# Optimization experiments

Hardware: AMD Instinct MI355X
Metric: run time of the kernel (lower is better)

The kernel has to match this reference:

```python
import jax, jax.numpy as jnp
import numpy as np

B, S, H = 16, 512, 768
NH, HD = 12, 64  # num heads, head dim


def setup_inputs() -> dict:
    key = jax.random.key(0)
    ks = jax.random.split(key, 7)
    std = 0.02
    return {
        "hidden_state": jax.random.normal(ks[0], (B, S, H), dtype=jnp.float32),
        "attention_mask": jnp.ones((B, S), dtype=jnp.float32),
        "Wq": jax.random.normal(ks[1], (H, H), dtype=jnp.float32) * std,
        "bq": jnp.zeros((H,), dtype=jnp.float32),
        "Wk": jax.random.normal(ks[2], (H, H), dtype=jnp.float32) * std,
        "bk": jnp.zeros((H,), dtype=jnp.float32),
        "Wv": jax.random.normal(ks[3], (H, H), dtype=jnp.float32) * std,
        "bv": jnp.zeros((H,), dtype=jnp.float32),
    }


def reference(hidden_state, attention_mask, Wq, bq, Wk, bk, Wv, bv):
    b, s, h = hidden_state.shape
    scale = 1.0 / jnp.sqrt(jnp.asarray(HD, hidden_state.dtype))

    def split_heads(x):  # [B,S,H] -> [B,NH,S,HD]
        return x.reshape(b, s, NH, HD).transpose(0, 2, 1, 3)

    q = split_heads(hidden_state @ Wq.T + bq)
    k = split_heads(hidden_state @ Wk.T + bk)
    v = split_heads(hidden_state @ Wv.T + bv)

    # [B,NH,S,S]
    scores = jnp.einsum("bhqd,bhkd->bhqk", q, k) * scale
    mask_add = (1.0 - attention_mask)[:, None, None, :] * -10000.0
    probs = jax.nn.softmax(scores + mask_add, axis=-1)
    # dropout is identity in eval / deterministic reference

    ctx = jnp.einsum("bhqk,bhkd->bhqd", probs, v)
    ctx = ctx.transpose(0, 2, 1, 3).reshape(b, s, NH * HD)
    return ctx, probs
```

## Files before the change

kernel.cpp:

```cpp
#include <hip/hip_runtime.h>

namespace {
constexpr int kB  = 16;
constexpr int kS  = 512;
constexpr int kH  = 768;
constexpr int kNH = 12;
constexpr int kHD = 64;
constexpr int kM  = kB * kS;
}

typedef __attribute__((ext_vector_type(8))) short  short8;
typedef __attribute__((ext_vector_type(4))) float  f32x4;
typedef __attribute__((ext_vector_type(4))) unsigned short us4;
typedef __attribute__((ext_vector_type(2))) unsigned int   u32x2;

__device__ __forceinline__ unsigned short f2bf(float x) {
    unsigned u = __float_as_uint(x);
    return (unsigned short)((u + 0x7FFFu + ((u >> 16) & 1u)) >> 16);
}

__device__ __forceinline__ unsigned pack_bf16(float lo, float hi) {
    return (unsigned)f2bf(lo) | ((unsigned)f2bf(hi) << 16);
}

__device__ __forceinline__ void load_lds16(const unsigned short* g, unsigned short* l) {
    __builtin_amdgcn_global_load_lds(
        (const __attribute__((address_space(1))) void*)g,
        (__attribute__((address_space(3))) void*)l,
        16, 0, 0);
}

__global__ __launch_bounds__(256) void cvt_all_kernel(
    const float* __restrict__ hidden, const float* __restrict__ Wq,
    const float* __restrict__ Wk, const float* __restrict__ Wv,
    unsigned short* __restrict__ hbf, unsigned short* __restrict__ wqb,
    unsigned short* __restrict__ wkb, unsigned short* __restrict__ wvb)
{
    const int nH4 = (kM * kH) / 4;
    const int nW4 = (kH * kH) / 4;
    int i = blockIdx.x * 256 + threadIdx.x;
    const float* src;
    unsigned short* dst;
    int off;
    if (i < nH4) {
        src = hidden; dst = hbf; off = i;
    } else {
        int j = i - nH4;
        int which = j / nW4;
        off = j - which * nW4;
        src = (which == 0) ? Wq : (which == 1) ? Wk : Wv;
        dst = (which == 0) ? wqb : (which == 1) ? wkb : wvb;
    }
    float4 v = reinterpret_cast<const float4*>(src)[off];
    us4 o;
    o.x = f2bf(v.x); o.y = f2bf(v.y); o.z = f2bf(v.z); o.w = f2bf(v.w);
    reinterpret_cast<us4*>(dst)[off] = o;
}

__global__ __launch_bounds__(256) void qkv_mfma_kernel(
    const unsigned short* __restrict__ hbf,
    const unsigned short* __restrict__ Wqb,
    const unsigned short* __restrict__ Wkb,
    const unsigned short* __restrict__ Wvb,
    const float* __restrict__ bq, const float* __restrict__ bk,
    const float* __restrict__ bv,
    unsigned short* __restrict__ qhi, unsigned short* __restrict__ qlo,
    unsigned short* __restrict__ khi, unsigned short* __restrict__ klo,
    unsigned short* __restrict__ vt)
{
    const int which = blockIdx.z;
    const unsigned short* W = (which == 0) ? Wqb : (which == 1) ? Wkb : Wvb;
    const float* bias       = (which == 0) ? bq  : (which == 1) ? bk  : bv;

    const int n0 = blockIdx.x * 128;
    const int m0 = blockIdx.y * 128;

    const int t    = threadIdx.x;
    const int lane = t & 63;
    const int w    = t >> 6;
    const int wm   = w >> 1;
    const int wn   = w & 1;

    __shared__ unsigned short As[128 * 64];
    __shared__ unsigned short Bs[128 * 64];

    f32x4 acc[4][4] = {};

    const int row8  = lane >> 3;
    const int sunit = (lane & 7) ^ row8;
    const unsigned short* gA = hbf + (size_t)(m0 + w * 32 + row8) * kH + sunit * 8;
    const unsigned short* gB = W   + (size_t)(n0 + w * 32 + row8) * kH + sunit * 8;

    const int frow = lane & 15;
    const int fk   = (lane >> 4) * 8;
    const int fswz = (frow & 7) << 3;

    for (int k0 = 0; k0 < kH; k0 += 64) {
#pragma unroll
        for (int i = 0; i < 4; ++i) {
            load_lds16(gA + k0 + (size_t)(8 * i) * kH, &As[(w * 32 + 8 * i) * 64]);
            load_lds16(gB + k0 + (size_t)(8 * i) * kH, &Bs[(w * 32 + 8 * i) * 64]);
        }
        __syncthreads();

        short8 af[2][4], bf[2][4];
#pragma unroll
        for (int kk = 0; kk < 2; ++kk) {
#pragma unroll
            for (int i = 0; i < 4; ++i)
                af[kk][i] = *reinterpret_cast<const short8*>(
                    &As[(wm * 64 + i * 16 + frow) * 64 + ((kk * 32 + fk) ^ fswz)]);
#pragma unroll
            for (int j = 0; j < 4; ++j)
                bf[kk][j] = *reinterpret_cast<const short8*>(
                    &Bs[(wn * 64 + j * 16 + frow) * 64 + ((kk * 32 + fk) ^ fswz)]);
        }
#pragma unroll
        for (int kk = 0; kk < 2; ++kk)
#pragma unroll
            for (int i = 0; i < 4; ++i)
#pragma unroll
                for (int j = 0; j < 4; ++j)
                    acc[i][j] = __builtin_amdgcn_mfma_f32_16x16x32_bf16(
                        af[kk][i], bf[kk][j], acc[i][j], 0, 0, 0);
        __syncthreads();
    }

    const int col = lane & 15;
    const int rq4 = (lane >> 4) << 2;

    if (which < 2) {
        unsigned short* ohi = which ? khi : qhi;
        unsigned short* olo = which ? klo : qlo;
#pragma unroll
        for (int j = 0; j < 4; ++j) {
            const int n  = n0 + wn * 64 + j * 16 + col;
            const float bj = bias[n];
            const int hh = n >> 6, d = n & 63;
#pragma unroll
            for (int i = 0; i < 4; ++i) {
                const int mrow = m0 + wm * 64 + i * 16 + rq4;
                const int bb = mrow >> 9;
                const int ss = mrow & 511;
                const size_t base =
                    ((size_t)(bb * kNH + hh) * kS + ss) * kHD + d;
#pragma unroll
                for (int r = 0; r < 4; ++r) {
                    float x = acc[i][j][r] + bj;
                    unsigned short hi = f2bf(x);
                    float res = x - __uint_as_float((unsigned)hi << 16);
                    ohi[base + (size_t)r * kHD] = hi;
                    olo[base + (size_t)r * kHD] = f2bf(res);
                }
            }
        }
    } else {
#pragma unroll
        for (int j = 0; j < 4; ++j) {
            const int n  = n0 + wn * 64 + j * 16 + col;
            const float bj = bias[n];
            const int hh = n >> 6, d = n & 63;
#pragma unroll
            for (int i = 0; i < 4; ++i) {
                const int mrow = m0 + wm * 64 + i * 16 + rq4;
                const int bb = mrow >> 9;
                const int ss = mrow & 511;
                us4 o;
                o.x = f2bf(acc[i][j][0] + bj);
                o.y = f2bf(acc[i][j][1] + bj);
                o.z = f2bf(acc[i][j][2] + bj);
                o.w = f2bf(acc[i][j][3] + bj);
                *reinterpret_cast<us4*>(
                    &vt[((size_t)(bb * kNH + hh) * kHD + d) * kS + ss]) = o;
            }
        }
    }
}

__global__ __launch_bounds__(256) void attn_kernel(
    const unsigned short* __restrict__ qhi, const unsigned short* __restrict__ qlo,
    const unsigned short* __restrict__ khi, const unsigned short* __restrict__ klo,
    const unsigned short* __restrict__ vtp, const float* __restrict__ mask,
    float* __restrict__ ctx, float* __restrict__ probs)
{
    const int bid = blockIdx.x;
    const int swz = (bid & 7) * 192 + (bid >> 3);
    const int qt  = swz & 7;
    const int bh  = swz >> 3;
    const int b   = bh / kNH;
    const int h   = bh % kNH;
    const int q0  = qt * 64;

    const int t    = threadIdx.x;
    const int lane = t & 63;
    const int w    = t >> 6;
    const int g    = lane >> 4;
    const int fr   = lane & 15;

    __shared__ unsigned short Khs[2][4096];
    __shared__ unsigned short Kls[2][4096];
    __shared__ unsigned short Vts[2][4096];
    __shared__ unsigned int   Pp[4][576];

    const int qrow = q0 + w * 16 + fr;
    const unsigned short* qh = qhi + ((size_t)bh * kS + qrow) * kHD + g * 8;
    const unsigned short* ql = qlo + ((size_t)bh * kS + qrow) * kHD + g * 8;
    const short8 qfh0 = *reinterpret_cast<const short8*>(qh);
    const short8 qfh1 = *reinterpret_cast<const short8*>(qh + 32);
    const short8 qfl0 = *reinterpret_cast<const short8*>(ql);
    const short8 qfl1 = *reinterpret_cast<const short8*>(ql + 32);

    const int c0 = (w * 2 + 0) * 64 + lane;
    const int c1 = (w * 2 + 1) * 64 + lane;
    const int r0 = c0 >> 3, r1 = c1 >> 3;
    const int s0b = ((c0 & 7) * 16) ^ ((r0 & 7) << 4);
    const int s1b = ((c1 & 7) * 16) ^ ((r1 & 7) << 4);
    const int ko0 = r0 * 128 + s0b,  ko1 = r1 * 128 + s1b;
    const int vo0 = r0 * 1024 + s0b, vo1 = r1 * 1024 + s1b;
    const char* kh_b = (const char*)(khi + (size_t)bh * kS * kHD);
    const char* kl_b = (const char*)(klo + (size_t)bh * kS * kHD);
    const char* vt_b = (const char*)(vtp + (size_t)bh * kHD * kS);
    const int l0 = (w * 2 + 0) * 512;
    const int l1 = (w * 2 + 1) * 512;

    unsigned pk[8][4][2];
    f32x4 cacc[4] = {};
    float rs = 0.0f;
    const float* mrow = mask + b * kS;

    load_lds16((const unsigned short*)(kh_b + ko0), &Khs[0][l0]);
    load_lds16((const unsigned short*)(kh_b + ko1), &Khs[0][l1]);
    load_lds16((const unsigned short*)(kl_b + ko0), &Kls[0][l0]);
    load_lds16((const unsigned short*)(kl_b + ko1), &Kls[0][l1]);
    load_lds16((const unsigned short*)(vt_b + vo0), &Vts[0][l0]);
    load_lds16((const unsigned short*)(vt_b + vo1), &Vts[0][l1]);

#pragma unroll
    for (int kt = 0; kt < 8; ++kt) {
        const int cur = kt & 1;
        __syncthreads();

        if (kt < 7) {
            const int nxt = cur ^ 1;
            load_lds16((const unsigned short*)(kh_b + (kt + 1) * 8192 + ko0), &Khs[nxt][l0]);
            load_lds16((const unsigned short*)(kh_b + (kt + 1) * 8192 + ko1), &Khs[nxt][l1]);
            load_lds16((const unsigned short*)(kl_b + (kt + 1) * 8192 + ko0), &Kls[nxt][l0]);
            load_lds16((const unsigned short*)(kl_b + (kt + 1) * 8192 + ko1), &Kls[nxt][l1]);
            load_lds16((const unsigned short*)(vt_b + (kt + 1) * 128 + vo0), &Vts[nxt][l0]);
            load_lds16((const unsigned short*)(vt_b + (kt + 1) * 128 + vo1), &Vts[nxt][l1]);
        }

        __builtin_amdgcn_s_setprio(1);

#pragma unroll
        for (int ks = 0; ks < 4; ++ks) {
            f32x4 sa = {};
#pragma unroll
            for (int d2 = 0; d2 < 2; ++d2) {
                const int kr  = ks * 16 + fr;
                const int off = kr * 128 + ((d2 * 64 + g * 16) ^ ((kr & 7) << 4));
                short8 ah = *reinterpret_cast<const short8*>((const char*)Khs[cur] + off);
                short8 al = *reinterpret_cast<const short8*>((const char*)Kls[cur] + off);
                const short8 qhf = d2 ? qfh1 : qfh0;
                const short8 qlf = d2 ? qfl1 : qfl0;
                sa = __builtin_amdgcn_mfma_f32_16x16x32_bf16(ah, qhf, sa, 0, 0, 0);
                sa = __builtin_amdgcn_mfma_f32_16x16x32_bf16(ah, qlf, sa, 0, 0, 0);
                sa = __builtin_amdgcn_mfma_f32_16x16x32_bf16(al, qhf, sa, 0, 0, 0);
            }
            const float4 mv = *reinterpret_cast<const float4*>(
                &mrow[kt * 64 + ks * 16 + g * 4]);
            float p0 = __expf(fmaf(sa[0], 0.125f, fmaf(mv.x, 1e4f, -1e4f)));
            float p1 = __expf(fmaf(sa[1], 0.125f, fmaf(mv.y, 1e4f, -1e4f)));
            float p2 = __expf(fmaf(sa[2], 0.125f, fmaf(mv.z, 1e4f, -1e4f)));
            float p3 = __expf(fmaf(sa[3], 0.125f, fmaf(mv.w, 1e4f, -1e4f)));
            rs += (p0 + p1) + (p2 + p3);
            const unsigned u0 = pack_bf16(p0, p1);
            const unsigned u1 = pack_bf16(p2, p3);
            pk[kt][ks][0] = u0;
            pk[kt][ks][1] = u1;
            *reinterpret_cast<u32x2*>(&Pp[w][fr * 36 + ks * 8 + g * 2]) =
                (u32x2){u0, u1};
        }

#pragma unroll
        for (int kp = 0; kp < 2; ++kp) {
            short8 pa = *reinterpret_cast<const short8*>(
                &Pp[w][fr * 36 + kp * 16 + g * 4]);
#pragma unroll
            for (int dt = 0; dt < 4; ++dt) {
                const int vr  = dt * 16 + fr;
                const int off = vr * 128 + ((kp * 64 + g * 16) ^ ((vr & 7) << 4));
                short8 vb = *reinterpret_cast<const short8*>((const char*)Vts[cur] + off);
                cacc[dt] = __builtin_amdgcn_mfma_f32_16x16x32_bf16(
                    pa, vb, cacc[dt], 0, 0, 0);
            }
        }

        __builtin_amdgcn_s_setprio(0);
    }

    rs += __shfl_xor(rs, 16, 64);
    rs += __shfl_xor(rs, 32, 64);
    const float inv = 1.0f / rs;

    float* prow = probs + ((size_t)bh * kS + qrow) * kS;
#pragma unroll
    for (int kt = 0; kt < 8; ++kt)
#pragma unroll
        for (int ks = 0; ks < 4; ++ks) {
            const unsigned u0 = pk[kt][ks][0], u1 = pk[kt][ks][1];
            f32x4 o;
            o.x = __uint_as_float(u0 << 16) * inv;
            o.y = __uint_as_float(u0 & 0xFFFF0000u) * inv;
            o.z = __uint_as_float(u1 << 16) * inv;
            o.w = __uint_as_float(u1 & 0xFFFF0000u) * inv;
            __builtin_nontemporal_store(
                o, reinterpret_cast<f32x4*>(prow + kt * 64 + ks * 16 + g * 4));
        }

    float invr[4];
#pragma unroll
    for (int r = 0; r < 4; ++r) invr[r] = __shfl(inv, g * 4 + r, 64);
    float* crow = ctx + ((size_t)(b * kS + q0 + w * 16 + g * 4)) * kH
                      + h * kHD + fr;
#pragma unroll
    for (int dt = 0; dt < 4; ++dt)
#pragma unroll
        for (int r = 0; r < 4; ++r)
            __builtin_nontemporal_store(cacc[dt][r] * invr[r],
                                        crow + (size_t)r * kH + dt * 16);
}

extern "C" void kernel_launch(void* const* d_in, const int* in_sizes, int n_in,
                              void* d_out, int out_size, void* d_ws, size_t ws_size,
                              hipStream_t stream) {
    (void)in_sizes; (void)n_in; (void)out_size; (void)ws_size;

    const float* hidden = (const float*)d_in[0];
    const float* mask   = (const float*)d_in[1];
    const float* Wq     = (const float*)d_in[2];
    const float* bq     = (const float*)d_in[3];
    const float* Wk     = (const float*)d_in[4];
    const float* bk     = (const float*)d_in[5];
    const float* Wv     = (const float*)d_in[6];
    const float* bv     = (const float*)d_in[7];

    float* ctx   = (float*)d_out;
    float* probs = (float*)d_out + (size_t)kB * kS * kH;

    unsigned short* hbf = (unsigned short*)d_ws;
    unsigned short* wqb = hbf + (size_t)kM * kH;
    unsigned short* wkb = wqb + (size_t)kH * kH;
    unsigned short* wvb = wkb + (size_t)kH * kH;
    unsigned short* qhi = wvb + (size_t)kH * kH;
    const size_t nqkv = (size_t)kB * kNH * kS * kHD;
    unsigned short* qlo = qhi + nqkv;
    unsigned short* khi = qlo + nqkv;
    unsigned short* klo = khi + nqkv;
    unsigned short* vt  = klo + nqkv;

    const int ncvt = ((kM * kH) / 4 + 3 * (kH * kH) / 4) / 256;
    cvt_all_kernel<<<ncvt, 256, 0, stream>>>(hidden, Wq, Wk, Wv,
                                             hbf, wqb, wkb, wvb);

    dim3 gp(kH / 128, kM / 128, 3);
    qkv_mfma_kernel<<<gp, 256, 0, stream>>>(hbf, wqb, wkb, wvb,
                                            bq, bk, bv,
                                            qhi, qlo, khi, klo, vt);

    attn_kernel<<<dim3(kB * kNH * (kS / 64)), 256, 0, stream>>>(
        qhi, qlo, khi, klo, vt, mask, ctx, probs);
}
```

Before: 383.7 us.

## Load K and V fragments directly from global memory instead of LDS staging

Removes the double-buffered LDS staging of K-hi, K-lo and V^T tiles along with the per-iteration block barrier. Each wave now reads its MFMA operand fragments straight from global memory (relying on L1/L2 for reuse across the four waves), and the launch bounds request two blocks per SIMD. This gets rid of the LDS traffic and the syncthreads, but every wave now re-fetches the same K/V data and global-load latency is exposed without explicit prefetch.

Result: slower. 487.6 us (+27.1%).

```diff
diff --git a/kernel.cpp b/kernel.cpp
--- a/kernel.cpp
+++ b/kernel.cpp
@@ -177,7 +177,7 @@
     }
 }
 
-__global__ __launch_bounds__(256) void attn_kernel(
+__global__ __launch_bounds__(256, 2) void attn_kernel(
     const unsigned short* __restrict__ qhi, const unsigned short* __restrict__ qlo,
     const unsigned short* __restrict__ khi, const unsigned short* __restrict__ klo,
     const unsigned short* __restrict__ vtp, const float* __restrict__ mask,
@@ -197,75 +197,47 @@
     const int g    = lane >> 4;
     const int fr   = lane & 15;
 
-    __shared__ unsigned short Khs[2][4096];
-    __shared__ unsigned short Kls[2][4096];
-    __shared__ unsigned short Vts[2][4096];
-    __shared__ unsigned int   Pp[4][576];
+    __shared__ unsigned int Pp[4][576];
 
     const int qrow = q0 + w * 16 + fr;
     const unsigned short* qh = qhi + ((size_t)bh * kS + qrow) * kHD + g * 8;
     const unsigned short* ql = qlo + ((size_t)bh * kS + qrow) * kHD + g * 8;
-    const short8 qfh0 = *reinterpret_cast<const short8*>(qh);
-    const short8 qfh1 = *reinterpret_cast<const short8*>(qh + 32);
-    const short8 qfl0 = *reinterpret_cast<const short8*>(ql);
-    const short8 qfl1 = *reinterpret_cast<const short8*>(ql + 32);
-
-    const int c0 = (w * 2 + 0) * 64 + lane;
-    const int c1 = (w * 2 + 1) * 64 + lane;
-    const int r0 = c0 >> 3, r1 = c1 >> 3;
-    const int s0b = ((c0 & 7) * 16) ^ ((r0 & 7) << 4);
-    const int s1b = ((c1 & 7) * 16) ^ ((r1 & 7) << 4);
-    const int ko0 = r0 * 128 + s0b,  ko1 = r1 * 128 + s1b;
-    const int vo0 = r0 * 1024 + s0b, vo1 = r1 * 1024 + s1b;
-    const char* kh_b = (const char*)(khi + (size_t)bh * kS * kHD);
-    const char* kl_b = (const char*)(klo + (size_t)bh * kS * kHD);
-    const char* vt_b = (const char*)(vtp + (size_t)bh * kHD * kS);
-    const int l0 = (w * 2 + 0) * 512;
-    const int l1 = (w * 2 + 1) * 512;
+    short8 qfh[2], qfl[2];
+    qfh[0] = *reinterpret_cast<const short8*>(qh);
+    qfh[1] = *reinterpret_cast<const short8*>(qh + 32);
+    qfl[0] = *reinterpret_cast<const short8*>(ql);
+    qfl[1] = *reinterpret_cast<const short8*>(ql + 32);
+
+    const unsigned short* kh_p = khi + (size_t)bh * kS * kHD + fr * kHD + g * 8;
+    const unsigned short* kl_p = klo + (size_t)bh * kS * kHD + fr * kHD + g * 8;
+    const unsigned short* vt_p = vtp + (size_t)bh * kHD * kS + fr * kS + g * 8;
 
     unsigned pk[8][4][2];
     f32x4 cacc[4] = {};
     float rs = 0.0f;
     const float* mrow = mask + b * kS;
 
-    load_lds16((const unsigned short*)(kh_b + ko0), &Khs[0][l0]);
-    load_lds16((const unsigned short*)(kh_b + ko1), &Khs[0][l1]);
-    load_lds16((const unsigned short*)(kl_b + ko0), &Kls[0][l0]);
-    load_lds16((const unsigned short*)(kl_b + ko1), &Kls[0][l1]);
-    load_lds16((const unsigned short*)(vt_b + vo0), &Vts[0][l0]);
-    load_lds16((const unsigned short*)(vt_b + vo1), &Vts[0][l1]);
-
 #pragma unroll
     for (int kt = 0; kt < 8; ++kt) {
-        const int cur = kt & 1;
-        __syncthreads();
-
-        if (kt < 7) {
-            const int nxt = cur ^ 1;
-            load_lds16((const unsigned short*)(kh_b + (kt + 1) * 8192 + ko0), &Khs[nxt][l0]);
-            load_lds16((const unsigned short*)(kh_b + (kt + 1) * 8192 + ko1), &Khs[nxt][l1]);
-            load_lds16((const unsigned short*)(kl_b + (kt + 1) * 8192 + ko0), &Kls[nxt][l0]);
-            load_lds16((const unsigned short*)(kl_b + (kt + 1) * 8192 + ko1), &Kls[nxt][l1]);
-            load_lds16((const unsigned short*)(vt_b + (kt + 1) * 128 + vo0), &Vts[nxt][l0]);
-            load_lds16((const unsigned short*)(vt_b + (kt + 1) * 128 + vo1), &Vts[nxt][l1]);
-        }
-
-        __builtin_amdgcn_s_setprio(1);
+        short8 vb[2][4];
+#pragma unroll
+        for (int kp = 0; kp < 2; ++kp)
+#pragma unroll
+            for (int dt = 0; dt < 4; ++dt)
+                vb[kp][dt] = *reinterpret_cast<const short8*>(
+                    vt_p + (size_t)dt * (16 * kS) + kt * 64 + kp * 32);
 
 #pragma unroll
         for (int ks = 0; ks < 4; ++ks) {
             f32x4 sa = {};
 #pragma unroll
             for (int d2 = 0; d2 < 2; ++d2) {
-                const int kr  = ks * 16 + fr;
-                const int off = kr * 128 + ((d2 * 64 + g * 16) ^ ((kr & 7) << 4));
-                short8 ah = *reinterpret_cast<const short8*>((const char*)Khs[cur] + off);
-                short8 al = *reinterpret_cast<const short8*>((const char*)Kls[cur] + off);
-                const short8 qhf = d2 ? qfh1 : qfh0;
-                const short8 qlf = d2 ? qfl1 : qfl0;
-                sa = __builtin_amdgcn_mfma_f32_16x16x32_bf16(ah, qhf, sa, 0, 0, 0);
-                sa = __builtin_amdgcn_mfma_f32_16x16x32_bf16(ah, qlf, sa, 0, 0, 0);
-                sa = __builtin_amdgcn_mfma_f32_16x16x32_bf16(al, qhf, sa, 0, 0, 0);
+                const size_t koff = (size_t)(kt * 64 + ks * 16) * kHD + d2 * 32;
+                short8 ah = *reinterpret_cast<const short8*>(kh_p + koff);
+                short8 al = *reinterpret_cast<const short8*>(kl_p + koff);
+                sa = __builtin_amdgcn_mfma_f32_16x16x32_bf16(ah, qfh[d2], sa, 0, 0, 0);
+                sa = __builtin_amdgcn_mfma_f32_16x16x32_bf16(ah, qfl[d2], sa, 0, 0, 0);
+                sa = __builtin_amdgcn_mfma_f32_16x16x32_bf16(al, qfh[d2], sa, 0, 0, 0);
             }
             const float4 mv = *reinterpret_cast<const float4*>(
                 &mrow[kt * 64 + ks * 16 + g * 4]);
@@ -287,16 +259,10 @@
             short8 pa = *reinterpret_cast<const short8*>(
                 &Pp[w][fr * 36 + kp * 16 + g * 4]);
 #pragma unroll
-            for (int dt = 0; dt < 4; ++dt) {
-                const int vr  = dt * 16 + fr;
-                const int off = vr * 128 + ((kp * 64 + g * 16) ^ ((vr & 7) << 4));
-                short8 vb = *reinterpret_cast<const short8*>((const char*)Vts[cur] + off);
+            for (int dt = 0; dt < 4; ++dt)
                 cacc[dt] = __builtin_amdgcn_mfma_f32_16x16x32_bf16(
-                    pa, vb, cacc[dt], 0, 0, 0);
-            }
-        }
-
-        __builtin_amdgcn_s_setprio(0);
+                    pa, vb[kp][dt], cacc[dt], 0, 0, 0);
+        }
     }
 
     rs += __shfl_xor(rs, 16, 64);
```
